# Optimization experiments

Hardware: AMD Instinct MI355X
Metric: run time of the kernel (lower is better)

The kernel has to match this reference:

```python
import jax, jax.numpy as jnp
import numpy as np

GROUP_MANTISSA = 8
GROUP_SIZE = 36


def bfp_quantize(x, mantissa=GROUP_MANTISSA, group_size=GROUP_SIZE):
    """Block floating point: flatten, group consecutive group_size elements,
    share the max exponent within each group, keep `mantissa` mantissa bits."""
    flat = x.reshape(-1)
    n = flat.shape[0]
    pad = (-n) % group_size
    f = jnp.pad(flat, (0, pad)).reshape(-1, group_size)  # [G, group_size]
    m = jnp.max(jnp.abs(f), axis=1, keepdims=True)       # group max magnitude
    safe_m = jnp.where(m > 0, m, jnp.ones_like(m))
    e = jnp.floor(jnp.log2(safe_m))                      # shared exponent
    scale = jnp.exp2(e - (mantissa - 1))                 # LSB step for the group
    q = jnp.round(f / scale) * scale
    q = jnp.where(m > 0, q, jnp.zeros_like(q))
    return q.reshape(-1)[:n].reshape(x.shape)


def setup_inputs() -> dict:
    key = jax.random.key(0)
    kx, kw, kb = jax.random.split(key, 3)
    x = jax.random.normal(kx, (32, 64, 112, 112), dtype=jnp.float32)
    # kaiming-uniform-ish scale for a 3x3x64 fan-in
    fan_in = 64 * 3 * 3
    bound = 1.0 / np.sqrt(fan_in)
    weight = jax.random.uniform(kw, (64, 64, 3, 3), dtype=jnp.float32, minval=-bound, maxval=bound) * np.sqrt(3.0)
    bias = jax.random.uniform(kb, (64,), dtype=jnp.float32, minval=-bound, maxval=bound)
    return {"x": x, "weight": weight, "bias": bias}


def reference(x, weight, bias):
    xq = bfp_quantize(x)
    wq = bfp_quantize(weight)
    out = jax.lax.conv_general_dilated(
        xq, wq,
        window_strides=(1, 1),
        padding=((1, 1), (1, 1)),
        lhs_dilation=(1, 1),
        rhs_dilation=(1, 1),
        dimension_numbers=("NCHW", "OIHW", "NCHW"),
        feature_group_count=1,
    )
    return out + bias[None, :, None, None]
```

## Files before the change

### kernel.cpp

```cpp
#include <hip/hip_runtime.h>

typedef __attribute__((ext_vector_type(4))) float f32x4;
typedef __attribute__((ext_vector_type(8))) short s16x8;
typedef __attribute__((ext_vector_type(4))) unsigned int u32x4;

#define HW 112
#define PW8 116
#define ROWS8 (PW8*8)
#define PLANE8 (112*ROWS8)
#define CHW (64*112*112)
#define NG 713615
#define X_F4 6422528

#define XQ8_BYTES 53215232
#define WT_OFF    53219328
#define SC_OFF    53293056
#define ZP_OFF    59001984

__device__ __forceinline__ unsigned short f32_to_bf16_exact(float q) {
    return (unsigned short)(__float_as_uint(q) >> 16);
}
__device__ __forceinline__ unsigned int pack_bf16x2(float a, float b) {
    return __builtin_amdgcn_perm(__float_as_uint(b), __float_as_uint(a), 0x07060302u);
}
__device__ __forceinline__ void scale_from_max(float m, float& scale, float& inv) {
    if (m > 0.f) {
        int e = (int)((__float_as_uint(m) >> 23) & 0xFF) - 127;
        scale = __builtin_ldexpf(1.0f, e - 7);
        inv   = __builtin_ldexpf(1.0f, 7 - e);
    } else { scale = 0.f; inv = 0.f; }
}

__global__ __launch_bounds__(256) void q1_scales(const float* __restrict__ x,
                                                 const float* __restrict__ w,
                                                 float2* __restrict__ sc,
                                                 unsigned short* __restrict__ wt,
                                                 u32x4* __restrict__ zp) {
    __shared__ float lmax[2304];
    const int b = blockIdx.x, tid = threadIdx.x;

    if (b == 2788) {
        if (tid < 64) zp[tid] = (u32x4){0u, 0u, 0u, 0u};
        #pragma unroll 1
        for (int rep = 0; rep < 4; ++rep) {
            int g = rep * 256 + tid;
            const float4* p = (const float4*)w + g * 9;
            float vv[36]; float m = 0.f;
            #pragma unroll
            for (int i = 0; i < 9; ++i) {
                float4 v = p[i];
                vv[i*4+0]=v.x; vv[i*4+1]=v.y; vv[i*4+2]=v.z; vv[i*4+3]=v.w;
                m = fmaxf(m, fmaxf(fmaxf(fabsf(v.x), fabsf(v.y)), fmaxf(fabsf(v.z), fabsf(v.w))));
            }
            float s, inv; scale_from_max(m, s, inv);
            #pragma unroll
            for (int j = 0; j < 36; ++j) {
                int flat = g * 36 + j;
                int k = flat / 576, rem = flat % 576;
                int c = rem / 9, pp = rem % 9;
                float q = rintf(vv[j] * inv) * s;
                wt[pp * 4096 + k * 64 + c] = f32_to_bf16_exact(q);
            }
        }
        return;
    }

    long base4 = (long)b * 2304;
    #pragma unroll
    for (int it = 0; it < 9; ++it) {
        int i = it * 256 + tid;
        long g4 = base4 + i;
        float m = 0.f;
        if (g4 < X_F4) {
            float4 v = ((const float4*)x)[g4];
            m = fmaxf(fmaxf(fabsf(v.x), fabsf(v.y)), fmaxf(fabsf(v.z), fabsf(v.w)));
        }
        lmax[i] = m;
    }
    __syncthreads();
    int g = b * 256 + tid;
    if (g < NG) {
        float m = 0.f; int o = tid * 9;
        #pragma unroll
        for (int j = 0; j < 9; ++j) m = fmaxf(m, lmax[o + j]);
        float s, inv; scale_from_max(m, s, inv);
        sc[g] = make_float2(s, inv);
    }
}

__global__ __launch_bounds__(256) void q2_quant(const float* __restrict__ x,
                                                const float2* __restrict__ sc,
                                                unsigned short* __restrict__ xq8) {
    int blk = blockIdx.x;
    int pb = blk % 49; int t2 = blk / 49; int oct = t2 & 7; int n = t2 >> 3;
    int p = pb * 256 + threadIdx.x;
    int h = p / 112, ww = p - h * 112;
    unsigned short* row = xq8 + ((n * 8 + oct) * 112 + h) * ROWS8;
    int cbase = (n * 64 + oct * 8) * 12544 + p;
    unsigned int pk[4];
    #pragma unroll
    for (int jj = 0; jj < 4; ++jj) {
        int f0 = cbase + (2 * jj) * 12544;
        int f1 = f0 + 12544;
        float2 s0 = sc[(unsigned)f0 / 36u];
        float2 s1 = sc[(unsigned)f1 / 36u];
        float q0 = rintf(x[f0] * s0.y) * s0.x;
        float q1 = rintf(x[f1] * s1.y) * s1.x;
        pk[jj] = pack_bf16x2(q0, q1);
    }
    *(u32x4*)(row + (ww + 2) * 8) = (u32x4){pk[0], pk[1], pk[2], pk[3]};
    u32x4 z4 = {0u, 0u, 0u, 0u};
    if (ww == 0)        { *(u32x4*)(row) = z4;            *(u32x4*)(row + 8) = z4; }
    else if (ww == 111) { *(u32x4*)(row + 114 * 8) = z4;  *(u32x4*)(row + 115 * 8) = z4; }
}

__global__ __launch_bounds__(256) void conv_mfma(const unsigned short* __restrict__ xq8,
                                                 const unsigned short* __restrict__ wt,
                                                 const float* __restrict__ bias,
                                                 float* __restrict__ out,
                                                 const unsigned short* __restrict__ zp) {
    __shared__ unsigned short xs[2][3328 * 8];
    const int tid = threadIdx.x;
    const int wave = tid >> 6, lane = tid & 63;
    const int wl = lane & 15, quad = lane >> 4;
    const int kg = wave & 1, mg = wave >> 1;
    const int bs = blockIdx.x;

    unsigned pk13[13];
    #pragma unroll
    for (int k = 0; k < 13; ++k) {
        int g = (wave * 13 + k) * 64 + lane;
        if (g < 3200) {
            int oct = g / 400, rem = g - oct * 400;
            int r = rem / 40, pix = rem - r * 40;
            int pixs = pix ^ oct;
            pk13[k] = ((unsigned)r << 24) | (unsigned)(oct * PLANE8 + pixs * 8);
        } else pk13[k] = 0xFF000000u;
    }

    float bv[2];
    #pragma unroll
    for (int j = 0; j < 2; ++j) bv[j] = bias[kg * 32 + j * 16 + wl];
    int pixb[7];
    #pragma unroll
    for (int mti = 0; mti < 7; ++mti) {
        int m = (mg * 7 + mti) * 16 + wl;
        pixb[mti] = (m / 28) * 40 + (m % 28) + 1;
    }

    auto issue = [&](int ti, int bi) {
        int t = bs + 256 * ti;
        int st = ((t & 7) * 224) + (t >> 3);
        int n = st / 56, rem = st - n * 56;
        int h0 = (rem >> 2) * 8, w0 = (rem & 3) * 28;
        const unsigned short* base = xq8 + n * 8 * PLANE8 + w0 * 8;
        #pragma unroll
        for (int k = 0; k < 13; ++k) {
            unsigned pk = pk13[k];
            int r = (int)(pk >> 24);
            int hh = h0 - 1 + r;
            bool ok = (r <= 9) && (hh >= 0) && (hh < HW);
            const unsigned short* src = ok ? (base + (pk & 0xFFFFFFu) + hh * ROWS8) : zp;
            unsigned short* dst = (unsigned short*)&xs[bi][(wave * 13 + k) * 512];
            __builtin_amdgcn_global_load_lds(
                (const __attribute__((address_space(1))) void*)src,
                (__attribute__((address_space(3))) void*)dst, 16, 0, 0);
        }
    };

    issue(0, 0);

    #pragma unroll 1
    for (int i = 0; i < 7; ++i) {
        asm volatile("s_waitcnt vmcnt(0)" ::: "memory");
        __builtin_amdgcn_s_barrier();
        if (i < 6) issue(i + 1, (i + 1) & 1);

        int t = bs + 256 * i;
        int st = ((t & 7) * 224) + (t >> 3);
        int n = st / 56, rem = st - n * 56;
        int h0 = (rem >> 2) * 8, w0 = (rem & 3) * 28;
        const unsigned short* xb = &xs[i & 1][0];

        f32x4 acc[7][2];
        f32x4 zero = {0.f, 0.f, 0.f, 0.f};
        #pragma unroll
        for (int mti = 0; mti < 7; ++mti) { acc[mti][0] = zero; acc[mti][1] = zero; }

        #pragma unroll
        for (int p = 0; p < 9; ++p) {
            const int dpix = (p / 3) * 40 + (p % 3);
            #pragma unroll
            for (int cs = 0; cs < 2; ++cs) {
                const int oq = cs * 4 + quad;
                s16x8 B0 = *(const s16x8*)(wt + p * 4096 + ((kg * 2 + 0) * 16 + wl) * 64 + cs * 32 + quad * 8);
                s16x8 B1 = *(const s16x8*)(wt + p * 4096 + ((kg * 2 + 1) * 16 + wl) * 64 + cs * 32 + quad * 8);
                s16x8 A[7];
                #pragma unroll
                for (int mti = 0; mti < 7; ++mti) {
                    int pix = pixb[mti] + dpix;
                    A[mti] = *(const s16x8*)(xb + (oq * 400 + (pix ^ oq)) * 8);
                }
                #pragma unroll
                for (int mti = 0; mti < 7; ++mti) {
                    acc[mti][0] = __builtin_amdgcn_mfma_f32_16x16x32_bf16(A[mti], B0, acc[mti][0], 0, 0, 0);
                    acc[mti][1] = __builtin_amdgcn_mfma_f32_16x16x32_bf16(A[mti], B1, acc[mti][1], 0, 0, 0);
                }
            }
        }

        int obase = n * CHW + h0 * HW + w0;
        #pragma unroll
        for (int mti = 0; mti < 7; ++mti) {
            int m0 = (mg * 7 + mti) * 16 + quad * 4;
            int eofs = (m0 / 28) * HW + (m0 % 28);
            #pragma unroll
            for (int j = 0; j < 2; ++j) {
                f32x4 v = acc[mti][j];
                v.x += bv[j]; v.y += bv[j]; v.z += bv[j]; v.w += bv[j];
                *(f32x4*)(out + obase + (kg * 32 + j * 16 + wl) * 12544 + eofs) = v;
            }
        }
    }
}

extern "C" void kernel_launch(void* const* d_in, const int* in_sizes, int n_in,
                              void* d_out, int out_size, void* d_ws, size_t ws_size,
                              hipStream_t stream) {
    const float* x    = (const float*)d_in[0];
    const float* w    = (const float*)d_in[1];
    const float* bias = (const float*)d_in[2];
    float* out = (float*)d_out;
    char* ws = (char*)d_ws;
    unsigned short* xq8 = (unsigned short*)ws;
    unsigned short* wt  = (unsigned short*)(ws + WT_OFF);
    float2*         sc  = (float2*)(ws + SC_OFF);
    unsigned short* zp  = (unsigned short*)(ws + ZP_OFF);

    hipLaunchKernelGGL(q1_scales, dim3(2789),  dim3(256), 0, stream, x, w, sc, wt, (u32x4*)zp);
    hipLaunchKernelGGL(q2_quant,  dim3(12544), dim3(256), 0, stream, x, sc, xq8);
    hipLaunchKernelGGL(conv_mfma, dim3(256),   dim3(256), 0, stream, xq8, wt, bias, out, zp);
}
```

Before: 273.1 us.

## Fuse activation BFP scale computation and quantization into one kernel

After: 253.1 us. 7.3% less time.

```diff
diff --git a/kernel.cpp b/kernel.cpp
--- a/kernel.cpp
+++ b/kernel.cpp
@@ -5,16 +5,12 @@
 typedef __attribute__((ext_vector_type(4))) unsigned int u32x4;
 
 #define HW 112
-#define PW8 116
-#define ROWS8 (PW8*8)
+#define ROWS8 (116*8)
 #define PLANE8 (112*ROWS8)
 #define CHW (64*112*112)
-#define NG 713615
-#define X_F4 6422528
-
-#define XQ8_BYTES 53215232
+#define X_ELEMS 25690112
+
 #define WT_OFF    53219328
-#define SC_OFF    53293056
 #define ZP_OFF    59001984
 
 __device__ __forceinline__ unsigned short f32_to_bf16_exact(float q) {
@@ -31,87 +27,100 @@
     } else { scale = 0.f; inv = 0.f; }
 }
 
-__global__ __launch_bounds__(256) void q1_scales(const float* __restrict__ x,
-                                                 const float* __restrict__ w,
-                                                 float2* __restrict__ sc,
+__global__ __launch_bounds__(256) void qw_kernel(const float* __restrict__ w,
                                                  unsigned short* __restrict__ wt,
                                                  u32x4* __restrict__ zp) {
-    __shared__ float lmax[2304];
-    const int b = blockIdx.x, tid = threadIdx.x;
-
-    if (b == 2788) {
-        if (tid < 64) zp[tid] = (u32x4){0u, 0u, 0u, 0u};
-        #pragma unroll 1
-        for (int rep = 0; rep < 4; ++rep) {
-            int g = rep * 256 + tid;
-            const float4* p = (const float4*)w + g * 9;
-            float vv[36]; float m = 0.f;
+    if (blockIdx.x == 0 && threadIdx.x < 64) zp[threadIdx.x] = (u32x4){0u, 0u, 0u, 0u};
+    int g = blockIdx.x * 256 + threadIdx.x;
+    const float4* p = (const float4*)w + g * 9;
+    float vv[36]; float m = 0.f;
+    #pragma unroll
+    for (int i = 0; i < 9; ++i) {
+        float4 v = p[i];
+        vv[i*4+0]=v.x; vv[i*4+1]=v.y; vv[i*4+2]=v.z; vv[i*4+3]=v.w;
+        m = fmaxf(m, fmaxf(fmaxf(fabsf(v.x), fabsf(v.y)), fmaxf(fabsf(v.z), fabsf(v.w))));
+    }
+    float s, inv; scale_from_max(m, s, inv);
+    #pragma unroll
+    for (int j = 0; j < 36; ++j) {
+        int flat = g * 36 + j;
+        int k = flat / 576, rem = flat % 576;
+        int c = rem / 9, pp = rem % 9;
+        float q = rintf(vv[j] * inv) * s;
+        wt[pp * 4096 + k * 64 + c] = f32_to_bf16_exact(q);
+    }
+}
+
+__global__ __launch_bounds__(256) void qx_fused(const float* __restrict__ x,
+                                                unsigned short* __restrict__ xq8) {
+    __shared__ float vals[8 * 448];
+    __shared__ float lmax[1024];
+    __shared__ float2 ssc[8][16];
+    __shared__ int sgs[8];
+    const int tid = threadIdx.x;
+    const int b = blockIdx.x;
+    const int plane = b / 28, chunk = b - plane * 28;
+    const int p0 = chunk * 448;
+    const int base_plane = plane * 8 * 12544;
+
+    #pragma unroll
+    for (int it = 0; it < 4; ++it) {
+        int g = it * 256 + tid;
+        int j = g >> 7, gi = g & 127;
+        int flat = base_plane + j * 12544 + p0 - 32 + gi * 4;
+        float4 v = {0.f, 0.f, 0.f, 0.f};
+        if (flat >= 0 && flat < X_ELEMS) v = *(const float4*)(x + flat);
+        lmax[g] = fmaxf(fmaxf(fabsf(v.x), fabsf(v.y)), fmaxf(fabsf(v.z), fabsf(v.w)));
+        if (gi >= 8 && gi < 120)
+            *(f32x4*)&vals[j * 448 + (gi - 8) * 4] = (f32x4){v.x, v.y, v.z, v.w};
+    }
+    __syncthreads();
+
+    if (tid < 128) {
+        int j = tid >> 4, k = tid & 15;
+        unsigned a0 = (unsigned)(base_plane + j * 12544 + p0);
+        int gstart = (int)(a0 / 36u);
+        int gend   = (int)((a0 + 447u) / 36u);
+        if (k == 0) sgs[j] = gstart;
+        if (gstart + k <= gend) {
+            int ps = 36 * (gstart + k) - (int)a0;
+            int gb = ps / 4 + 8;
+            float m = 0.f;
             #pragma unroll
-            for (int i = 0; i < 9; ++i) {
-                float4 v = p[i];
-                vv[i*4+0]=v.x; vv[i*4+1]=v.y; vv[i*4+2]=v.z; vv[i*4+3]=v.w;
-                m = fmaxf(m, fmaxf(fmaxf(fabsf(v.x), fabsf(v.y)), fmaxf(fabsf(v.z), fabsf(v.w))));
+            for (int q = 0; q < 9; ++q) m = fmaxf(m, lmax[j * 128 + gb + q]);
+            float s, inv; scale_from_max(m, s, inv);
+            ssc[j][k] = make_float2(s, inv);
+        }
+    }
+    __syncthreads();
+
+    const int hrow0 = chunk * 4;
+    #pragma unroll
+    for (int it = 0; it < 2; ++it) {
+        int s = it * 256 + tid;
+        if (s < 464) {
+            int h = s / 116, w = s - h * 116;
+            unsigned short* dst = xq8 + (plane * 112 + hrow0 + h) * ROWS8 + w * 8;
+            u32x4 o = {0u, 0u, 0u, 0u};
+            if (w >= 2 && w < 114) {
+                int dp = h * 112 + (w - 2);
+                unsigned pbase = (unsigned)(base_plane + p0 + dp);
+                float qv[8];
+                #pragma unroll
+                for (int j = 0; j < 8; ++j) {
+                    float v = vals[j * 448 + dp];
+                    unsigned g = (pbase + (unsigned)j * 12544u) / 36u;
+                    float2 sv = ssc[j][(int)g - sgs[j]];
+                    qv[j] = rintf(v * sv.y) * sv.x;
+                }
+                o.x = pack_bf16x2(qv[0], qv[1]);
+                o.y = pack_bf16x2(qv[2], qv[3]);
+                o.z = pack_bf16x2(qv[4], qv[5]);
+                o.w = pack_bf16x2(qv[6], qv[7]);
             }
-            float s, inv; scale_from_max(m, s, inv);
-            #pragma unroll
-            for (int j = 0; j < 36; ++j) {
-                int flat = g * 36 + j;
-                int k = flat / 576, rem = flat % 576;
-                int c = rem / 9, pp = rem % 9;
-                float q = rintf(vv[j] * inv) * s;
-                wt[pp * 4096 + k * 64 + c] = f32_to_bf16_exact(q);
-            }
-        }
-        return;
-    }
-
-    long base4 = (long)b * 2304;
-    #pragma unroll
-    for (int it = 0; it < 9; ++it) {
-        int i = it * 256 + tid;
-        long g4 = base4 + i;
-        float m = 0.f;
-        if (g4 < X_F4) {
-            float4 v = ((const float4*)x)[g4];
-            m = fmaxf(fmaxf(fabsf(v.x), fabsf(v.y)), fmaxf(fabsf(v.z), fabsf(v.w)));
-        }
-        lmax[i] = m;
-    }
-    __syncthreads();
-    int g = b * 256 + tid;
-    if (g < NG) {
-        float m = 0.f; int o = tid * 9;
-        #pragma unroll
-        for (int j = 0; j < 9; ++j) m = fmaxf(m, lmax[o + j]);
-        float s, inv; scale_from_max(m, s, inv);
-        sc[g] = make_float2(s, inv);
-    }
-}
-
-__global__ __launch_bounds__(256) void q2_quant(const float* __restrict__ x,
-                                                const float2* __restrict__ sc,
-                                                unsigned short* __restrict__ xq8) {
-    int blk = blockIdx.x;
-    int pb = blk % 49; int t2 = blk / 49; int oct = t2 & 7; int n = t2 >> 3;
-    int p = pb * 256 + threadIdx.x;
-    int h = p / 112, ww = p - h * 112;
-    unsigned short* row = xq8 + ((n * 8 + oct) * 112 + h) * ROWS8;
-    int cbase = (n * 64 + oct * 8) * 12544 + p;
-    unsigned int pk[4];
-    #pragma unroll
-    for (int jj = 0; jj < 4; ++jj) {
-        int f0 = cbase + (2 * jj) * 12544;
-        int f1 = f0 + 12544;
-        float2 s0 = sc[(unsigned)f0 / 36u];
-        float2 s1 = sc[(unsigned)f1 / 36u];
-        float q0 = rintf(x[f0] * s0.y) * s0.x;
-        float q1 = rintf(x[f1] * s1.y) * s1.x;
-        pk[jj] = pack_bf16x2(q0, q1);
-    }
-    *(u32x4*)(row + (ww + 2) * 8) = (u32x4){pk[0], pk[1], pk[2], pk[3]};
-    u32x4 z4 = {0u, 0u, 0u, 0u};
-    if (ww == 0)        { *(u32x4*)(row) = z4;            *(u32x4*)(row + 8) = z4; }
-    else if (ww == 111) { *(u32x4*)(row + 114 * 8) = z4;  *(u32x4*)(row + 115 * 8) = z4; }
+            *(u32x4*)dst = o;
+        }
+    }
 }
 
 __global__ __launch_bounds__(256) void conv_mfma(const unsigned short* __restrict__ xq8,
@@ -234,10 +243,9 @@
     char* ws = (char*)d_ws;
     unsigned short* xq8 = (unsigned short*)ws;
     unsigned short* wt  = (unsigned short*)(ws + WT_OFF);
-    float2*         sc  = (float2*)(ws + SC_OFF);
     unsigned short* zp  = (unsigned short*)(ws + ZP_OFF);
 
-    hipLaunchKernelGGL(q1_scales, dim3(2789),  dim3(256), 0, stream, x, w, sc, wt, (u32x4*)zp);
-    hipLaunchKernelGGL(q2_quant,  dim3(12544), dim3(256), 0, stream, x, sc, xq8);
-    hipLaunchKernelGGL(conv_mfma, dim3(256),   dim3(256), 0, stream, xq8, wt, bias, out, zp);
-}
+    hipLaunchKernelGGL(qw_kernel, dim3(4),    dim3(256), 0, stream, w, wt, (u32x4*)zp);
+    hipLaunchKernelGGL(qx_fused,  dim3(7168), dim3(256), 0, stream, x, xq8);
+    hipLaunchKernelGGL(conv_mfma, dim3(256),  dim3(256), 0, stream, xq8, wt, bias, out, zp);
+}
```
